# Kernel tuning notes

Hardware: AMD Instinct MI355X
Metric: run time of the kernel (lower is better)

The kernel has to match this reference:

```python
import jax, jax.numpy as jnp
from jax import lax
import numpy as np


def _edt_to(zero_mask):
    """Exact Euclidean distance from every pixel to the nearest True pixel of
    zero_mask. Equivalent to scipy.ndimage.distance_transform_edt(~zero_mask).
    Separable two-pass algorithm: 1-D distance along W (two scans), then an
    exact lower-envelope min along H using squared distances.
    zero_mask: bool [B, H, W] -> float32 [B, H, W].
    """
    B, H, W = zero_mask.shape
    INF = jnp.float32(H + W)  # larger than any attainable 1-D distance
    bg = jnp.transpose(zero_mask, (2, 0, 1))  # [W, B, H]: scan over W

    def step(c, b):
        c = jnp.where(b, 0.0, c + 1.0)
        return c, c

    init = jnp.full((B, H), INF, dtype=jnp.float32)
    _, f = lax.scan(step, init, bg)                 # left-to-right
    _, r = lax.scan(step, init, bg, reverse=True)   # right-to-left
    d1 = jnp.minimum(f, r)                          # [W, B, H] 1-D dist along W
    g = jnp.transpose(d1 * d1, (1, 2, 0))           # [B, H, W] squared 1-D dist

    # d2[b, y, x] = min_{y'} g[b, y', x] + (y - y')^2   (exact 2-D squared EDT)
    yy = jnp.arange(H, dtype=jnp.float32)
    dy2 = (yy[:, None] - yy[None, :]) ** 2          # [H, H']
    d2 = jnp.min(g[:, None, :, :] + dy2[None, :, :, None], axis=2)  # [B, H, W]
    return jnp.sqrt(d2)


def _boundary_loss(preds, targets, idx_class=None):
    B, C, H, W = preds.shape
    probs = jax.nn.softmax(preds, axis=1)
    classes = [idx_class] if idx_class is not None else list(range(1, C))
    total = jnp.float32(0.0)
    count = jnp.float32(0.0)
    for cls in classes:
        pos = targets == cls        # bool [B, H, W]
        neg = ~pos
        has = jnp.any(pos)
        # scipy: distance(negmask)*negmask - (distance(posmask)-1)*posmask
        # distance_transform_edt(negmask) == dist to nearest pos pixel, etc.
        dmap = _edt_to(pos) * neg - (_edt_to(neg) - 1.0) * pos
        loss = jnp.mean(dmap * probs[:, cls])
        total = total + jnp.where(has, loss, 0.0)
        count = count + has.astype(jnp.float32)
    return jnp.where(count > 0, total / jnp.maximum(count, 1.0), jnp.float32(0.0))


def setup_inputs() -> dict:
    key = jax.random.key(0)
    k1, k2 = jax.random.split(key)
    preds = jax.random.normal(k1, (8, 4, 256, 256), dtype=jnp.float32)
    targets = jax.random.randint(k2, (8, 256, 256), 0, 4)
    return {"preds": preds, "targets": targets}


def reference(preds, targets):
    return _boundary_loss(preds, targets, idx_class=None)
```

## Files before the change

kernel.cpp:

```cpp
#include <hip/hip_runtime.h>
#include <math.h>

#define BB 8
#define HH 256
#define WW 256
#define T  4
#define NW 4
#define PAD 96
#define LDSW (WW + 2 * PAD)

typedef unsigned long long u64;

__global__ __launch_bounds__(128) void build_masks(const int* __restrict__ tgt,
                                                   unsigned short* __restrict__ masks16,
                                                   float* __restrict__ out) {
  const int tx = threadIdx.x;
  const int xh = blockIdx.x & 1;
  const int b  = blockIdx.x >> 1;
  const int w  = blockIdx.y;
  const int q  = blockIdx.z;
  const int x  = xh * 128 + tx;
  if (b == 0 && w == 0 && q == 0 && x == 0) out[0] = 0.0f;
  unsigned m0 = 0, m1 = 0, m2 = 0, m3 = 0, bit = 1u;
  const int* p = tgt + ((size_t)b * HH + w * 64 + q * 16) * WW + x;
  for (int r = 0; r < 16; ++r, bit += bit) {
    int e = p[r * WW];
    m0 |= (e == 0) ? bit : 0u;
    m1 |= (e == 1) ? bit : 0u;
    m2 |= (e == 2) ? bit : 0u;
    m3 |= (e == 3) ? bit : 0u;
  }
  unsigned short* mp = masks16 + (((size_t)(b * NW + w) * WW + x) * 4) * 4 + q;
  mp[0]  = (unsigned short)m0;
  mp[4]  = (unsigned short)m1;
  mp[8]  = (unsigned short)m2;
  mp[12] = (unsigned short)m3;
}

__global__ __launch_bounds__(256, 2) void fused(const u64* __restrict__ masks,
                                                const float* __restrict__ preds,
                                                float* __restrict__ out) {
  __shared__ float g[T][LDSW][4];
  __shared__ float fred[4];
  const int x  = threadIdx.x;
  const int b  = blockIdx.x;
  const int y0 = blockIdx.y * T;
  const int wy = y0 >> 6;

  u64 m[NW][4];
  {
    const u64* mb = masks + ((size_t)b * NW * WW + x) * 4;
#pragma unroll
    for (int w = 0; w < NW; ++w) {
      ulonglong2 lo = *(const ulonglong2*)(mb + (size_t)w * WW * 4 + 0);
      ulonglong2 hi = *(const ulonglong2*)(mb + (size_t)w * WW * 4 + 2);
      m[w][0] = lo.x; m[w][1] = lo.y; m[w][2] = hi.x; m[w][3] = hi.y;
    }
  }

  float pr[T][4];
#pragma unroll
  for (int j = 0; j < T; ++j) {
    const float* pb = preds + ((size_t)b * 4 * HH + (y0 + j)) * WW + x;
    pr[j][0] = pb[0 * HH * WW];
    pr[j][1] = pb[1 * HH * WW];
    pr[j][2] = pb[2 * HH * WW];
    pr[j][3] = pb[3 * HH * WW];
  }

  for (int i = x; i < T * 2 * PAD; i += 256) {
    int j = i / (2 * PAD);
    int q = i - j * (2 * PAD);
    int idx = (q < PAD) ? q : (q + WW);
    *(float4*)&g[j][idx][0] = make_float4(1e30f, 1e30f, 1e30f, 1e30f);
  }

  int posmax[4] = {-4096, -4096, -4096, -4096};
  int posmin[4] = { 8192,  8192,  8192,  8192};
#pragma unroll
  for (int w = 0; w < NW; ++w) {
    if (w < wy) {
#pragma unroll
      for (int k = 0; k < 4; ++k) {
        u64 bits = m[w][k];
        int pos = w * 64 + 63 - __clzll((long long)bits);
        posmax[k] = max(posmax[k], bits ? pos : -4096);
      }
    } else if (w > wy) {
#pragma unroll
      for (int k = 0; k < 4; ++k) {
        u64 bits = m[w][k];
        int pos = w * 64 + (__ffsll((long long)bits) - 1);
        posmin[k] = min(posmin[k], bits ? pos : 8192);
      }
    }
  }

  float d[T][4];
  int lmax = 0;
#pragma unroll
  for (int j = 0; j < T; ++j) {
    const int y  = y0 + j;
    const int ly = y & 63;
    const int ini = min(513 + y, 768 - y);
    float4 gv;
    float* gp_ = (float*)&gv;
#pragma unroll
    for (int k = 0; k < 4; ++k) {
      u64 bits = m[wy][k];
      u64 lo = bits & ((2ull << ly) - 1ull);
      u64 hi = bits >> ly;
      int dl = ly - 63 + __clzll((long long)lo);
      int dh = __ffsll((long long)hi) - 1;
      int best = min(ini, y - posmax[k]);
      best = min(best, posmin[k] - y);
      best = min(best, lo ? dl : 1024);
      best = min(best, hi ? dh : 1024);
      lmax = max(lmax, best);
      float fb = (float)(best * best);
      gp_[k] = fb;
      d[j][k] = fb;
    }
    *(float4*)&g[j][x + PAD][0] = gv;
  }

#pragma unroll
  for (int off = 32; off; off >>= 1) lmax = max(lmax, __shfl_xor(lmax, off, 64));
  const int R  = __builtin_amdgcn_readfirstlane(lmax);
  const int Rw = min(R, PAD);
  __syncthreads();

  float mydone = 0.0f;
#pragma unroll
  for (int j = 0; j < T; ++j)
    mydone = fmaxf(mydone,
                   fmaxf(fmaxf(d[j][0], d[j][1]), fmaxf(d[j][2], d[j][3])));

  bool alldone = false;
  for (int kk = 1; kk <= Rw; ++kk) {
    float fkk = (float)kk;
    float fk2 = fkk * fkk;
    bool act = (mydone > fk2);
    if (__all(!act)) { alldone = true; break; }
    if (act) {
#pragma unroll
      for (int j = 0; j < T; ++j) {
        float4 gm = *(const float4*)&g[j][x + PAD - kk][0];
        float4 gq = *(const float4*)&g[j][x + PAD + kk][0];
        d[j][0] = fminf(d[j][0], fminf(gm.x, gq.x) + fk2);
        d[j][1] = fminf(d[j][1], fminf(gm.y, gq.y) + fk2);
        d[j][2] = fminf(d[j][2], fminf(gm.z, gq.z) + fk2);
        d[j][3] = fminf(d[j][3], fminf(gm.w, gq.w) + fk2);
      }
      float md = 0.0f;
#pragma unroll
      for (int j = 0; j < T; ++j)
        md = fmaxf(md, fmaxf(fmaxf(d[j][0], d[j][1]), fmaxf(d[j][2], d[j][3])));
      mydone = md;
    }
  }
  if (!alldone && R > PAD) {
#pragma unroll 1
    for (int kk = PAD + 1; kk <= R; ++kk) {
      float fkk = (float)kk;
      float fk2 = fkk * fkk;
      bool act = (mydone > fk2);
      if (__all(!act)) break;
      if (act) {
        int xm = max(x - kk, 0), xp = min(x + kk, WW - 1);
        float dm = (float)(x - xm), dpq = (float)(xp - x);
        float dm2 = dm * dm, dp2 = dpq * dpq;
#pragma unroll
        for (int j = 0; j < T; ++j) {
          float4 gm = *(const float4*)&g[j][xm + PAD][0];
          float4 gq = *(const float4*)&g[j][xp + PAD][0];
          d[j][0] = fminf(d[j][0], fminf(gm.x + dm2, gq.x + dp2));
          d[j][1] = fminf(d[j][1], fminf(gm.y + dm2, gq.y + dp2));
          d[j][2] = fminf(d[j][2], fminf(gm.z + dm2, gq.z + dp2));
          d[j][3] = fminf(d[j][3], fminf(gm.w + dm2, gq.w + dp2));
        }
        float md = 0.0f;
#pragma unroll
        for (int j = 0; j < T; ++j)
          md = fmaxf(md, fmaxf(fmaxf(d[j][0], d[j][1]), fmaxf(d[j][2], d[j][3])));
        mydone = md;
      }
    }
  }

  float acc = 0.0f;
#pragma unroll
  for (int j = 0; j < T; ++j) {
    const int ly = (y0 + j) & 63;
    const int t = (int)((m[wy][1] >> ly) & 1ull) * 1 +
                  (int)((m[wy][2] >> ly) & 1ull) * 2 +
                  (int)((m[wy][3] >> ly) & 1ull) * 3;
    float p0 = pr[j][0], p1 = pr[j][1], p2 = pr[j][2], p3 = pr[j][3];
    float pm = fmaxf(fmaxf(p0, p1), fmaxf(p2, p3));
    float e0 = expf(p0 - pm), e1 = expf(p1 - pm);
    float e2 = expf(p2 - pm), e3 = expf(p3 - pm);
    float inv = 1.0f / (e0 + e1 + e2 + e3);

    float dn1 = fminf(d[j][0], fminf(d[j][2], d[j][3]));
    float dn2 = fminf(d[j][0], fminf(d[j][1], d[j][3]));
    float dn3 = fminf(d[j][0], fminf(d[j][1], d[j][2]));
    float c1 = (t == 1) ? (1.0f - sqrtf(dn1)) : sqrtf(d[j][1]);
    float c2 = (t == 2) ? (1.0f - sqrtf(dn2)) : sqrtf(d[j][2]);
    float c3 = (t == 3) ? (1.0f - sqrtf(dn3)) : sqrtf(d[j][3]);
    acc += (c1 * e1 + c2 * e2 + c3 * e3) * inv;
  }

#pragma unroll
  for (int off = 32; off; off >>= 1) acc += __shfl_down(acc, off, 64);
  if ((x & 63) == 0) fred[x >> 6] = acc;
  __syncthreads();
  if (x == 0)
    atomicAdd(out, (fred[0] + fred[1] + fred[2] + fred[3]) *
                       (1.0f / (3.0f * BB * HH * WW)));
}

extern "C" void kernel_launch(void* const* d_in, const int* in_sizes, int n_in,
                              void* d_out, int out_size, void* d_ws, size_t ws_size,
                              hipStream_t stream) {
  const float* preds = (const float*)d_in[0];
  const int*   tgt   = (const int*)d_in[1];
  float* out   = (float*)d_out;
  u64*   masks = (u64*)d_ws;

  build_masks<<<dim3(BB * 2, NW, 4), 128, 0, stream>>>(tgt, (unsigned short*)masks, out);
  fused<<<dim3(BB, HH / T), 256, 0, stream>>>(masks, preds, out);
}
```

Measured before the change: 72.72 us.

## Merge mask build and fused EDT into one cooperative kernel with grid sync

The separate mask-building kernel and the fused distance/loss kernel are combined into a single cooperative launch of 512 blocks. The first 256 blocks build per-class bitmasks (now written as bytes over 8-row octets), then a grid-wide sync is taken before every block runs the EDT and loss computation. This removes one kernel launch and the gap between launches, at the cost of a cooperative grid barrier and byte-granular scattered stores to the mask buffer.

```diff
diff --git a/kernel.cpp b/kernel.cpp
--- a/kernel.cpp
+++ b/kernel.cpp
@@ -1,4 +1,5 @@
 #include <hip/hip_runtime.h>
+#include <hip/hip_cooperative_groups.h>
 #include <math.h>
 
 #define BB 8
@@ -11,40 +12,43 @@
 
 typedef unsigned long long u64;
 
-__global__ __launch_bounds__(128) void build_masks(const int* __restrict__ tgt,
-                                                   unsigned short* __restrict__ masks16,
-                                                   float* __restrict__ out) {
-  const int tx = threadIdx.x;
-  const int xh = blockIdx.x & 1;
-  const int b  = blockIdx.x >> 1;
-  const int w  = blockIdx.y;
-  const int q  = blockIdx.z;
-  const int x  = xh * 128 + tx;
-  if (b == 0 && w == 0 && q == 0 && x == 0) out[0] = 0.0f;
-  unsigned m0 = 0, m1 = 0, m2 = 0, m3 = 0, bit = 1u;
-  const int* p = tgt + ((size_t)b * HH + w * 64 + q * 16) * WW + x;
-  for (int r = 0; r < 16; ++r, bit += bit) {
-    int e = p[r * WW];
-    m0 |= (e == 0) ? bit : 0u;
-    m1 |= (e == 1) ? bit : 0u;
-    m2 |= (e == 2) ? bit : 0u;
-    m3 |= (e == 3) ? bit : 0u;
-  }
-  unsigned short* mp = masks16 + (((size_t)(b * NW + w) * WW + x) * 4) * 4 + q;
-  mp[0]  = (unsigned short)m0;
-  mp[4]  = (unsigned short)m1;
-  mp[8]  = (unsigned short)m2;
-  mp[12] = (unsigned short)m3;
-}
-
-__global__ __launch_bounds__(256, 2) void fused(const u64* __restrict__ masks,
-                                                const float* __restrict__ preds,
-                                                float* __restrict__ out) {
+__global__ __launch_bounds__(256, 2) void mega(const int* __restrict__ tgt,
+                                               const float* __restrict__ preds,
+                                               u64* __restrict__ masks,
+                                               float* __restrict__ out) {
   __shared__ float g[T][LDSW][4];
   __shared__ float fred[4];
+
+  if (blockIdx.x == 0 && threadIdx.x == 0) out[0] = 0.0f;
+  if (blockIdx.x < 256) {
+    const int item = blockIdx.x * 256 + threadIdx.x;
+    const int bx = item & 255;
+    const int h  = (item >> 8) & 31;
+    const int bb = item >> 13;
+    const int w  = h >> 3;
+    const int oct = h & 7;
+    const int* p = tgt + ((size_t)bb * HH + h * 8) * WW + bx;
+    unsigned c0 = 0, c1 = 0, c2 = 0, c3 = 0, bit = 1u;
+    for (int r = 0; r < 8; ++r, bit += bit) {
+      int e = p[r * WW];
+      c0 |= (e == 0) ? bit : 0u;
+      c1 |= (e == 1) ? bit : 0u;
+      c2 |= (e == 2) ? bit : 0u;
+      c3 |= (e == 3) ? bit : 0u;
+    }
+    unsigned char* m8 = (unsigned char*)masks;
+    const size_t u64idx = ((size_t)(bb * NW + w) * WW + bx) * 4;
+    m8[(u64idx + 0) * 8 + oct] = (unsigned char)c0;
+    m8[(u64idx + 1) * 8 + oct] = (unsigned char)c1;
+    m8[(u64idx + 2) * 8 + oct] = (unsigned char)c2;
+    m8[(u64idx + 3) * 8 + oct] = (unsigned char)c3;
+  }
+
+  cooperative_groups::this_grid().sync();
+
   const int x  = threadIdx.x;
-  const int b  = blockIdx.x;
-  const int y0 = blockIdx.y * T;
+  const int b  = blockIdx.x >> 6;
+  const int y0 = (blockIdx.x & 63) * T;
   const int wy = y0 >> 6;
 
   u64 m[NW][4];
@@ -227,6 +231,7 @@
   float* out   = (float*)d_out;
   u64*   masks = (u64*)d_ws;
 
-  build_masks<<<dim3(BB * 2, NW, 4), 128, 0, stream>>>(tgt, (unsigned short*)masks, out);
-  fused<<<dim3(BB, HH / T), 256, 0, stream>>>(masks, preds, out);
+  void* args[] = {(void*)&tgt, (void*)&preds, (void*)&masks, (void*)&out};
+  hipLaunchCooperativeKernel((const void*)mega, dim3(BB * (HH / T)), dim3(256),
+                             args, 0, stream);
 }
```

New measurement: 127.0 us. +74.7%, slower.

## Split class channels across two thread halves in fused EDT kernel

Applied to the files above, without the earlier changes.

The fused kernel now launches 512 threads per block. Each half of the block handles two of the four class masks for every column, which halves the per-thread register state and the LDS reads in the distance min-loop. After the loop, the per-class distances are written back to LDS and the rows are redistributed so each half computes the loss for two of the four rows. This adds a barrier plus LDS traffic for the exchange. Each half-wave's early-exit test now looks only at its two classes, so divergence and loop trip counts change.

```diff
diff --git a/kernel.cpp b/kernel.cpp
--- a/kernel.cpp
+++ b/kernel.cpp
@@ -37,58 +37,62 @@
   mp[12] = (unsigned short)m3;
 }
 
-__global__ __launch_bounds__(256, 2) void fused(const u64* __restrict__ masks,
+__global__ __launch_bounds__(512, 4) void fused(const u64* __restrict__ masks,
                                                 const float* __restrict__ preds,
                                                 float* __restrict__ out) {
   __shared__ float g[T][LDSW][4];
-  __shared__ float fred[4];
-  const int x  = threadIdx.x;
+  __shared__ u64 mws[WW][4];
+  __shared__ float fred[8];
+  const int tid = threadIdx.x;
+  const int x  = tid & 255;
+  const int h  = tid >> 8;
   const int b  = blockIdx.x;
   const int y0 = blockIdx.y * T;
   const int wy = y0 >> 6;
 
-  u64 m[NW][4];
+  u64 m[NW][2];
   {
-    const u64* mb = masks + ((size_t)b * NW * WW + x) * 4;
+    const u64* mb = masks + ((size_t)b * NW * WW + x) * 4 + 2 * h;
 #pragma unroll
     for (int w = 0; w < NW; ++w) {
-      ulonglong2 lo = *(const ulonglong2*)(mb + (size_t)w * WW * 4 + 0);
-      ulonglong2 hi = *(const ulonglong2*)(mb + (size_t)w * WW * 4 + 2);
-      m[w][0] = lo.x; m[w][1] = lo.y; m[w][2] = hi.x; m[w][3] = hi.y;
-    }
-  }
-
-  float pr[T][4];
-#pragma unroll
-  for (int j = 0; j < T; ++j) {
-    const float* pb = preds + ((size_t)b * 4 * HH + (y0 + j)) * WW + x;
-    pr[j][0] = pb[0 * HH * WW];
-    pr[j][1] = pb[1 * HH * WW];
-    pr[j][2] = pb[2 * HH * WW];
-    pr[j][3] = pb[3 * HH * WW];
-  }
-
-  for (int i = x; i < T * 2 * PAD; i += 256) {
+      ulonglong2 v = *(const ulonglong2*)(mb + (size_t)w * WW * 4);
+      m[w][0] = v.x; m[w][1] = v.y;
+    }
+  }
+  mws[x][2 * h]     = m[wy][0];
+  mws[x][2 * h + 1] = m[wy][1];
+
+  float pr[2][4];
+#pragma unroll
+  for (int jj = 0; jj < 2; ++jj) {
+    const float* pb = preds + ((size_t)b * 4 * HH + (y0 + 2 * h + jj)) * WW + x;
+    pr[jj][0] = pb[0 * HH * WW];
+    pr[jj][1] = pb[1 * HH * WW];
+    pr[jj][2] = pb[2 * HH * WW];
+    pr[jj][3] = pb[3 * HH * WW];
+  }
+
+  for (int i = tid; i < T * 2 * PAD; i += 512) {
     int j = i / (2 * PAD);
     int q = i - j * (2 * PAD);
     int idx = (q < PAD) ? q : (q + WW);
     *(float4*)&g[j][idx][0] = make_float4(1e30f, 1e30f, 1e30f, 1e30f);
   }
 
-  int posmax[4] = {-4096, -4096, -4096, -4096};
-  int posmin[4] = { 8192,  8192,  8192,  8192};
+  int posmax[2] = {-4096, -4096};
+  int posmin[2] = { 8192,  8192};
 #pragma unroll
   for (int w = 0; w < NW; ++w) {
     if (w < wy) {
 #pragma unroll
-      for (int k = 0; k < 4; ++k) {
+      for (int k = 0; k < 2; ++k) {
         u64 bits = m[w][k];
         int pos = w * 64 + 63 - __clzll((long long)bits);
         posmax[k] = max(posmax[k], bits ? pos : -4096);
       }
     } else if (w > wy) {
 #pragma unroll
-      for (int k = 0; k < 4; ++k) {
+      for (int k = 0; k < 2; ++k) {
         u64 bits = m[w][k];
         int pos = w * 64 + (__ffsll((long long)bits) - 1);
         posmin[k] = min(posmin[k], bits ? pos : 8192);
@@ -96,17 +100,16 @@
     }
   }
 
-  float d[T][4];
+  float d[T][2];
   int lmax = 0;
 #pragma unroll
   for (int j = 0; j < T; ++j) {
     const int y  = y0 + j;
     const int ly = y & 63;
     const int ini = min(513 + y, 768 - y);
-    float4 gv;
-    float* gp_ = (float*)&gv;
-#pragma unroll
-    for (int k = 0; k < 4; ++k) {
+    float2 gv;
+#pragma unroll
+    for (int k = 0; k < 2; ++k) {
       u64 bits = m[wy][k];
       u64 lo = bits & ((2ull << ly) - 1ull);
       u64 hi = bits >> ly;
@@ -118,10 +121,10 @@
       best = min(best, hi ? dh : 1024);
       lmax = max(lmax, best);
       float fb = (float)(best * best);
-      gp_[k] = fb;
+      ((float*)&gv)[k] = fb;
       d[j][k] = fb;
     }
-    *(float4*)&g[j][x + PAD][0] = gv;
+    *(float2*)&g[j][x + PAD][2 * h] = gv;
   }
 
 #pragma unroll
@@ -133,8 +136,7 @@
   float mydone = 0.0f;
 #pragma unroll
   for (int j = 0; j < T; ++j)
-    mydone = fmaxf(mydone,
-                   fmaxf(fmaxf(d[j][0], d[j][1]), fmaxf(d[j][2], d[j][3])));
+    mydone = fmaxf(mydone, fmaxf(d[j][0], d[j][1]));
 
   bool alldone = false;
   for (int kk = 1; kk <= Rw; ++kk) {
@@ -145,17 +147,15 @@
     if (act) {
 #pragma unroll
       for (int j = 0; j < T; ++j) {
-        float4 gm = *(const float4*)&g[j][x + PAD - kk][0];
-        float4 gq = *(const float4*)&g[j][x + PAD + kk][0];
+        float2 gm = *(const float2*)&g[j][x + PAD - kk][2 * h];
+        float2 gq = *(const float2*)&g[j][x + PAD + kk][2 * h];
         d[j][0] = fminf(d[j][0], fminf(gm.x, gq.x) + fk2);
         d[j][1] = fminf(d[j][1], fminf(gm.y, gq.y) + fk2);
-        d[j][2] = fminf(d[j][2], fminf(gm.z, gq.z) + fk2);
-        d[j][3] = fminf(d[j][3], fminf(gm.w, gq.w) + fk2);
       }
       float md = 0.0f;
 #pragma unroll
       for (int j = 0; j < T; ++j)
-        md = fmaxf(md, fmaxf(fmaxf(d[j][0], d[j][1]), fmaxf(d[j][2], d[j][3])));
+        md = fmaxf(md, fmaxf(d[j][0], d[j][1]));
       mydone = md;
     }
   }
@@ -172,51 +172,59 @@
         float dm2 = dm * dm, dp2 = dpq * dpq;
 #pragma unroll
         for (int j = 0; j < T; ++j) {
-          float4 gm = *(const float4*)&g[j][xm + PAD][0];
-          float4 gq = *(const float4*)&g[j][xp + PAD][0];
+          float2 gm = *(const float2*)&g[j][xm + PAD][2 * h];
+          float2 gq = *(const float2*)&g[j][xp + PAD][2 * h];
           d[j][0] = fminf(d[j][0], fminf(gm.x + dm2, gq.x + dp2));
           d[j][1] = fminf(d[j][1], fminf(gm.y + dm2, gq.y + dp2));
-          d[j][2] = fminf(d[j][2], fminf(gm.z + dm2, gq.z + dp2));
-          d[j][3] = fminf(d[j][3], fminf(gm.w + dm2, gq.w + dp2));
         }
         float md = 0.0f;
 #pragma unroll
         for (int j = 0; j < T; ++j)
-          md = fmaxf(md, fmaxf(fmaxf(d[j][0], d[j][1]), fmaxf(d[j][2], d[j][3])));
+          md = fmaxf(md, fmaxf(d[j][0], d[j][1]));
         mydone = md;
       }
     }
   }
 
+  __syncthreads();
+#pragma unroll
+  for (int j = 0; j < T; ++j)
+    *(float2*)&g[j][x + PAD][2 * h] = make_float2(d[j][0], d[j][1]);
+  __syncthreads();
+
   float acc = 0.0f;
 #pragma unroll
-  for (int j = 0; j < T; ++j) {
+  for (int jj = 0; jj < 2; ++jj) {
+    const int j  = 2 * h + jj;
     const int ly = (y0 + j) & 63;
-    const int t = (int)((m[wy][1] >> ly) & 1ull) * 1 +
-                  (int)((m[wy][2] >> ly) & 1ull) * 2 +
-                  (int)((m[wy][3] >> ly) & 1ull) * 3;
-    float p0 = pr[j][0], p1 = pr[j][1], p2 = pr[j][2], p3 = pr[j][3];
+    const int t = (int)((mws[x][1] >> ly) & 1ull) * 1 +
+                  (int)((mws[x][2] >> ly) & 1ull) * 2 +
+                  (int)((mws[x][3] >> ly) & 1ull) * 3;
+    float4 dj = *(const float4*)&g[j][x + PAD][0];
+    float p0 = pr[jj][0], p1 = pr[jj][1], p2 = pr[jj][2], p3 = pr[jj][3];
     float pm = fmaxf(fmaxf(p0, p1), fmaxf(p2, p3));
     float e0 = expf(p0 - pm), e1 = expf(p1 - pm);
     float e2 = expf(p2 - pm), e3 = expf(p3 - pm);
     float inv = 1.0f / (e0 + e1 + e2 + e3);
 
-    float dn1 = fminf(d[j][0], fminf(d[j][2], d[j][3]));
-    float dn2 = fminf(d[j][0], fminf(d[j][1], d[j][3]));
-    float dn3 = fminf(d[j][0], fminf(d[j][1], d[j][2]));
-    float c1 = (t == 1) ? (1.0f - sqrtf(dn1)) : sqrtf(d[j][1]);
-    float c2 = (t == 2) ? (1.0f - sqrtf(dn2)) : sqrtf(d[j][2]);
-    float c3 = (t == 3) ? (1.0f - sqrtf(dn3)) : sqrtf(d[j][3]);
+    float dn1 = fminf(dj.x, fminf(dj.z, dj.w));
+    float dn2 = fminf(dj.x, fminf(dj.y, dj.w));
+    float dn3 = fminf(dj.x, fminf(dj.y, dj.z));
+    float c1 = (t == 1) ? (1.0f - sqrtf(dn1)) : sqrtf(dj.y);
+    float c2 = (t == 2) ? (1.0f - sqrtf(dn2)) : sqrtf(dj.z);
+    float c3 = (t == 3) ? (1.0f - sqrtf(dn3)) : sqrtf(dj.w);
     acc += (c1 * e1 + c2 * e2 + c3 * e3) * inv;
   }
 
 #pragma unroll
   for (int off = 32; off; off >>= 1) acc += __shfl_down(acc, off, 64);
-  if ((x & 63) == 0) fred[x >> 6] = acc;
-  __syncthreads();
-  if (x == 0)
-    atomicAdd(out, (fred[0] + fred[1] + fred[2] + fred[3]) *
-                       (1.0f / (3.0f * BB * HH * WW)));
+  if ((tid & 63) == 0) fred[tid >> 6] = acc;
+  __syncthreads();
+  if (tid == 0) {
+    float s = fred[0] + fred[1] + fred[2] + fred[3] +
+              fred[4] + fred[5] + fred[6] + fred[7];
+    atomicAdd(out, s * (1.0f / (3.0f * BB * HH * WW)));
+  }
 }
 
 extern "C" void kernel_launch(void* const* d_in, const int* in_sizes, int n_in,
@@ -228,5 +236,5 @@
   u64*   masks = (u64*)d_ws;
 
   build_masks<<<dim3(BB * 2, NW, 4), 128, 0, stream>>>(tgt, (unsigned short*)masks, out);
-  fused<<<dim3(BB, HH / T), 256, 0, stream>>>(masks, preds, out);
+  fused<<<dim3(BB, HH / T), 512, 0, stream>>>(masks, preds, out);
 }
```

Result: no change. 72.86 us (+0.2%).
